# Kernel optimization log

Measured on AMD Instinct MI355X. Metric: run time of the kernel, lower is better.

The kernel has to match this reference:

```python
import jax, jax.numpy as jnp
import numpy as np

B, TQ, TK = 2, 2048, 2048
H, E, D = 16, 256, 4096       # num_heads, embed_dim, d_model
DH = D // H                   # head_dim == embed_dim (required by per-head RMSNorm(embed_dim))
LAMBDA_INIT = 0.8
LAYER_INDEX = 0
EPS = 1.1920929e-07           # torch RMSNorm default eps = finfo(float32).eps


def setup_inputs() -> dict:
    key = jax.random.key(0)
    ks = jax.random.split(key, 14)
    s = 0.02
    lam_init_val = LAMBDA_INIT - 0.6 * float(np.exp(-0.3 * LAYER_INDEX))
    return {
        "x": jax.random.normal(ks[0], (B, TQ, E), jnp.float32),
        "encoder_out": jax.random.normal(ks[1], (B, TK, E), jnp.float32),
        "Wq": jax.random.normal(ks[2], (H, E, DH), jnp.float32) * s,
        "bq": jnp.zeros((H, DH), jnp.float32),
        "Wk": jax.random.normal(ks[3], (H, E, DH), jnp.float32) * s,
        "bk": jnp.zeros((H, DH), jnp.float32),
        "Wv": jax.random.normal(ks[4], (H, E, DH), jnp.float32) * s,
        "bv": jnp.zeros((H, DH), jnp.float32),
        "lq1": jax.random.normal(ks[5], (H, DH), jnp.float32) * 0.1,
        "lk1": jax.random.normal(ks[6], (H, DH), jnp.float32) * 0.1,
        "lq2": jax.random.normal(ks[7], (H, DH), jnp.float32) * 0.1,
        "lk2": jax.random.normal(ks[8], (H, DH), jnp.float32) * 0.1,
        "lam_init": jnp.full((H,), lam_init_val, jnp.float32),
        "g": jnp.ones((H, DH), jnp.float32),     # per-head RMSNorm weight
        "Wo": jax.random.normal(ks[9], (D, E), jnp.float32) * s,
        "bo": jnp.zeros((E,), jnp.float32),
    }


def reference(x, encoder_out, Wq, bq, Wk, bk, Wv, bv,
              lq1, lk1, lq2, lk2, lam_init, g, Wo, bo):
    # per-head projections, vectorized over heads: [B,H,T,DH]
    q = jnp.einsum('bte,hed->bhtd', x, Wq) + bq[:, None, :]
    k = jnp.einsum('bse,hed->bhsd', encoder_out, Wk) + bk[:, None, :]
    v = jnp.einsum('bse,hed->bhsd', encoder_out, Wv) + bv[:, None, :]
    dh2 = DH // 2
    q1, q2 = q[..., :dh2], q[..., dh2:]
    k1, k2 = k[..., :dh2], k[..., dh2:]
    scale = 1.0 / jnp.sqrt(jnp.float32(dh2))
    s1 = jax.nn.softmax(jnp.einsum('bhtd,bhsd->bhts', q1, k1) * scale, axis=-1)
    s2 = jax.nn.softmax(jnp.einsum('bhtd,bhsd->bhts', q2, k2) * scale, axis=-1)
    # learned per-head lambda scalar
    lam = jnp.exp(jnp.sum(lq1 * lk1, axis=-1)) - jnp.exp(jnp.sum(lq2 * lk2, axis=-1)) + lam_init  # [H]
    w = s1 - lam[None, :, None, None] * s2
    o = jnp.einsum('bhts,bhsd->bhtd', w, v)
    # per-head RMSNorm + (1 - lambda_init) scaling
    rms = jnp.sqrt(jnp.mean(o * o, axis=-1, keepdims=True) + EPS)
    o = (1.0 - LAMBDA_INIT) * (o / rms) * g[None, :, None, :]
    # concat heads -> output projection
    o = o.transpose(0, 2, 1, 3).reshape(B, TQ, D)
    return o @ Wo + bo
```

## Files before the change

### kernel.cpp

```cpp
#include <hip/hip_runtime.h>
#include <hip/hip_bf16.h>
#include <stdint.h>
#include <math.h>

typedef __bf16 bf16;
typedef __bf16 bf16x8 __attribute__((ext_vector_type(8)));
typedef float f32x4 __attribute__((ext_vector_type(4)));
typedef float f32x16 __attribute__((ext_vector_type(16)));
typedef unsigned int u32;

#define MFMA16(a, b, c) __builtin_amdgcn_mfma_f32_16x16x32_bf16(a, b, c, 0, 0, 0)
#define MFMA32(a, b, c) __builtin_amdgcn_mfma_f32_32x32x16_bf16(a, b, c, 0, 0, 0)

typedef const u32 __attribute__((address_space(1)))* gptr1;
typedef u32 __attribute__((address_space(3)))* lptr3;

__device__ __forceinline__ void load_lds16(const void* g, void* l) {
    __builtin_amdgcn_global_load_lds((gptr1)g, (lptr3)l, 16, 0, 0);
}

__device__ __forceinline__ u32 pk2(float lo, float hi_) {
    union { bf16 h[2]; u32 u; } t;
    t.h[0] = (bf16)lo; t.h[1] = (bf16)hi_;
    return t.u;
}

#define SCALE_QK 0.08838834764831845f
#define LOG2E 1.4426950408889634f
#define QK_PRESCALE (SCALE_QK * LOG2E)
#define RMS_EPS 1.1920929e-07f
#define OUT_SCALE 0.2f
#define M0_BIAS (-16.0f)

__global__ __launch_bounds__(256) void prep(
    const float* __restrict__ x, const float* __restrict__ enc,
    bf16* __restrict__ xb, bf16* __restrict__ eb,
    const float* __restrict__ Wq, const float* __restrict__ Wk, const float* __restrict__ Wv,
    bf16* __restrict__ WTq, bf16* __restrict__ WTk, bf16* __restrict__ WTv,
    const float* __restrict__ Wo, bf16* __restrict__ WoT,
    const float* __restrict__ lq1, const float* __restrict__ lk1,
    const float* __restrict__ lq2, const float* __restrict__ lk2,
    const float* __restrict__ lam_init, float* __restrict__ lam_out) {
    __shared__ bf16 T[64][68];
    int bid = blockIdx.x, tid = threadIdx.x;

    if (bid < 1024) {
        int gid = bid * 256 + tid;
        const float* src = (gid < 131072) ? x : enc;
        bf16* dst = (gid < 131072) ? xb : eb;
        int i = (gid & 131071) * 8;
        float4 v0 = *(const float4*)(src + i);
        float4 v1 = *(const float4*)(src + i + 4);
        union { bf16 h[8]; uint4 u; } p;
        p.h[0] = (bf16)v0.x; p.h[1] = (bf16)v0.y; p.h[2] = (bf16)v0.z; p.h[3] = (bf16)v0.w;
        p.h[4] = (bf16)v1.x; p.h[5] = (bf16)v1.y; p.h[6] = (bf16)v1.z; p.h[7] = (bf16)v1.w;
        *(uint4*)(dst + i) = p.u;
        return;
    }
    if (bid < 1792) {
        int idx = bid - 1024;
        int z = idx >> 4, rem = idx & 15;
        int by = rem >> 2, bx = rem & 3;
        int iw = z >> 4, hh = z & 15;
        const float* src = (iw == 0 ? Wq : iw == 1 ? Wk : Wv) + hh * 65536;
        bf16* dst = (iw == 0 ? WTq : iw == 1 ? WTk : WTv) + hh * 65536;
        int r0 = by * 64, c0 = bx * 64;
#pragma unroll
        for (int t = 0; t < 4; ++t) {
            int idx2 = tid + t * 256;
            int row = idx2 >> 4, c4 = (idx2 & 15) * 4;
            float4 v = *(const float4*)(src + (r0 + row) * 256 + c0 + c4);
            T[row][c4] = (bf16)v.x; T[row][c4 + 1] = (bf16)v.y;
            T[row][c4 + 2] = (bf16)v.z; T[row][c4 + 3] = (bf16)v.w;
        }
        __syncthreads();
#pragma unroll
        for (int t = 0; t < 2; ++t) {
            int idx2 = tid + t * 256;
            int crow = idx2 >> 3, r8 = (idx2 & 7) * 8;
            union { bf16 h[8]; uint4 u; } p;
#pragma unroll
            for (int j = 0; j < 8; ++j) p.h[j] = T[r8 + j][crow];
            *(uint4*)(dst + (c0 + crow) * 256 + r0 + r8) = p.u;
        }
        return;
    }
    if (bid < 2048) {
        int idx = bid - 1792;
        int by = idx >> 2, bx = idx & 3;
        int r0 = by * 64, c0 = bx * 64;
#pragma unroll
        for (int t = 0; t < 4; ++t) {
            int idx2 = tid + t * 256;
            int row = idx2 >> 4, c4 = (idx2 & 15) * 4;
            float4 v = *(const float4*)(Wo + (size_t)(r0 + row) * 256 + c0 + c4);
            T[row][c4] = (bf16)v.x; T[row][c4 + 1] = (bf16)v.y;
            T[row][c4 + 2] = (bf16)v.z; T[row][c4 + 3] = (bf16)v.w;
        }
        __syncthreads();
#pragma unroll
        for (int t = 0; t < 2; ++t) {
            int idx2 = tid + t * 256;
            int crow = idx2 >> 3, r8 = (idx2 & 7) * 8;
            union { bf16 h[8]; uint4 u; } p;
#pragma unroll
            for (int j = 0; j < 8; ++j) p.h[j] = T[r8 + j][crow];
            *(uint4*)(WoT + (size_t)(c0 + crow) * 4096 + r0 + r8) = p.u;
        }
        return;
    }
    {
        int hh = tid >> 4, i = tid & 15;
        float s1 = 0.f, s2 = 0.f;
#pragma unroll
        for (int j = 0; j < 16; ++j) {
            int d = i + j * 16;
            s1 += lq1[hh * 256 + d] * lk1[hh * 256 + d];
            s2 += lq2[hh * 256 + d] * lk2[hh * 256 + d];
        }
#pragma unroll
        for (int msk = 1; msk < 16; msk <<= 1) { s1 += __shfl_xor(s1, msk); s2 += __shfl_xor(s2, msk); }
        if (i == 0) lam_out[hh] = __expf(s1) - __expf(s2) + lam_init[hh];
    }
}

__global__ __launch_bounds__(256) void proj_gemm(
    const bf16* __restrict__ xb, const bf16* __restrict__ eb,
    const bf16* __restrict__ WTq, const bf16* __restrict__ WTk, const bf16* __restrict__ WTv,
    const float* __restrict__ bq, const float* __restrict__ bk, const float* __restrict__ bv,
    bf16* __restrict__ Qb, bf16* __restrict__ Kb, bf16* __restrict__ VTb) {
    int z = blockIdx.z;
    const bf16* A = (z == 0) ? xb : eb;
    const bf16* BT = (z == 0) ? WTq : (z == 1) ? WTk : WTv;
    const float* bias = (z == 0) ? bq : (z == 1) ? bk : bv;
    bf16* out = (z == 0) ? Qb : Kb;
    float qs = (z == 0) ? QK_PRESCALE : 1.0f;

    __shared__ alignas(16) bf16 As[128 * 64];
    __shared__ alignas(16) bf16 Bs[128 * 64];
    int m0 = blockIdx.x * 128, n0 = blockIdx.y * 128;
    int tid = threadIdx.x, w = tid >> 6, lane = tid & 63;
    int lrow = lane & 15, lgrp = lane >> 4;
    int wr = (w >> 1) * 64, wc = (w & 1) * 64;

    f32x4 acc[4][4];
#pragma unroll
    for (int i = 0; i < 4; ++i)
#pragma unroll
        for (int j = 0; j < 4; ++j) acc[i][j] = (f32x4){0.f, 0.f, 0.f, 0.f};

    for (int k0 = 0; k0 < 256; k0 += 64) {
        __syncthreads();
#pragma unroll
        for (int t = 0; t < 4; ++t) {
            int s = tid + t * 256;
            int row = s >> 3;
            int cg = (s & 7) ^ (row & 7);
            load_lds16(A + (size_t)(m0 + row) * 256 + k0 + cg * 8, &As[s * 8]);
            load_lds16(BT + (size_t)(n0 + row) * 256 + k0 + cg * 8, &Bs[s * 8]);
        }
        __syncthreads();
#pragma unroll
        for (int ks = 0; ks < 2; ++ks) {
            bf16x8 af[4], bfr[4];
#pragma unroll
            for (int f = 0; f < 4; ++f) {
                int ra = wr + f * 16 + lrow;
                int rb = wc + f * 16 + lrow;
                af[f]  = *(const bf16x8*)&As[ra * 64 + (((ks * 4 + lgrp) ^ (ra & 7)) << 3)];
                bfr[f] = *(const bf16x8*)&Bs[rb * 64 + (((ks * 4 + lgrp) ^ (rb & 7)) << 3)];
            }
#pragma unroll
            for (int i = 0; i < 4; ++i)
#pragma unroll
                for (int j = 0; j < 4; ++j) acc[i][j] = MFMA16(af[i], bfr[j], acc[i][j]);
        }
    }

    if (z == 2) {
        int lg2 = ((lgrp & 1) << 1) | (lgrp >> 1);
#pragma unroll
        for (int i = 0; i < 4; ++i) {
            int m_ = m0 + wr + i * 16;
            int bb = m_ >> 11, tb = m_ & 2047;
#pragma unroll
            for (int j = 0; j < 4; ++j) {
                int n = n0 + wc + j * 16 + lrow;
                float bvv = bias[n];
                int hh = n >> 8, d = n & 255;
                union { bf16 h[4]; uint2 u2; } pk;
#pragma unroll
                for (int r = 0; r < 4; ++r) pk.h[r] = (bf16)(acc[i][j][r] + bvv);
                *(uint2*)(VTb + (((size_t)bb * 16 + hh) * 256 + d) * 2048 + tb + lg2 * 4) = pk.u2;
            }
        }
    } else {
#pragma unroll
        for (int i = 0; i < 4; ++i) {
#pragma unroll
            for (int j = 0; j < 4; ++j) {
                int n = n0 + wc + j * 16 + lrow;
                float bvv = bias[n];
                int hh = n >> 8, d = n & 255;
#pragma unroll
                for (int r = 0; r < 4; ++r) {
                    int m = m0 + wr + i * 16 + lgrp * 4 + r;
                    int bb = m >> 11, tt = m & 2047;
                    out[(((size_t)bb * 16 + hh) * 2048 + tt) * 256 + d] = (bf16)((acc[i][j][r] + bvv) * qs);
                }
            }
        }
    }
}

__global__ __launch_bounds__(256, 2) void attn_kernel(
    const bf16* __restrict__ Qb, const bf16* __restrict__ Kb, const bf16* __restrict__ VTb,
    const float* __restrict__ lam_ws, const float* __restrict__ g, bf16* __restrict__ On) {
    __shared__ alignas(16) char SMEM[75264];
    bf16* KsB = (bf16*)SMEM;
    bf16* VsB = (bf16*)(SMEM + 32768);
    float* o2buf  = (float*)SMEM;
    float* smem_i = (float*)(SMEM + 65536);
    float* smem_r = (float*)(SMEM + 66048);
    float* psum   = (float*)(SMEM + 66560);

    int orig = blockIdx.x;
    int xcd = orig & 7, idx = orig >> 3;
    int bh = xcd * 4 + (idx >> 5);
    int qb = idx & 31;
    int b = bh >> 4, h = bh & 15;
    int q0 = qb * 64;

    int tid = threadIdx.x, w = tid >> 6, lane = tid & 63;
    int lq = lane & 31, hi = lane >> 5;
    int br = w >> 1, qw = (w & 1) * 32;
    int ksw = lq & 7;
    int vsw = (lq >> 1) & 3;

    const bf16* Qg = Qb + ((size_t)bh * 2048 + q0 + qw + lq) * 256 + br * 128;
    bf16x8 qf[8];
#pragma unroll
    for (int dk = 0; dk < 8; ++dk)
        qf[dk] = *(const bf16x8*)(Qg + dk * 16 + hi * 8);

    f32x16 o[8];
#pragma unroll
    for (int dt = 0; dt < 8; ++dt)
#pragma unroll
        for (int i = 0; i < 16; ++i) o[dt][i] = 0.f;
    float lsum = 0.f;

    const bf16* Kg = Kb + (size_t)bh * 2048 * 256;
    const bf16* VTg = VTb + (size_t)bh * 256 * 2048;

    auto STAGE = [&](int buf, int kt) {
        int s0 = kt * 32;
#pragma unroll
        for (int i = 0; i < 4; ++i) {
            int s = i * 256 + tid;
            int row = s >> 5;
            int cg = (s & 31) ^ (row & 7);
            load_lds16(Kg + (size_t)(s0 + row) * 256 + cg * 8, KsB + buf * 8192 + s * 8);
        }
#pragma unroll
        for (int i = 0; i < 4; ++i) {
            int s = i * 256 + tid;
            int row = s >> 2;
            int cg = (s & 3) ^ ((row >> 1) & 3);
            load_lds16(VTg + (size_t)row * 2048 + s0 + cg * 8, VsB + buf * 8192 + s * 8);
        }
    };

    STAGE(0, 0);
    __syncthreads();

    int cur = 0;
    for (int kt = 0; kt < 64; ++kt) {
        if (kt + 1 < 64) STAGE(cur ^ 1, kt + 1);
        const bf16* Kbuf = KsB + cur * 8192;
        const bf16* Vbuf = VsB + cur * 8192;

        f32x16 sa, sb;
#pragma unroll
        for (int i = 0; i < 16; ++i) { sa[i] = M0_BIAS; sb[i] = 0.f; }
        __builtin_amdgcn_s_setprio(1);
#pragma unroll
        for (int dk = 0; dk < 4; ++dk) {
            bf16x8 k0 = *(const bf16x8*)&Kbuf[lq * 256 + (((br * 16 + 4 * dk + hi) ^ ksw) << 3)];
            bf16x8 k1 = *(const bf16x8*)&Kbuf[lq * 256 + (((br * 16 + 4 * dk + 2 + hi) ^ ksw) << 3)];
            sa = MFMA32(k0, qf[2 * dk], sa);
            sb = MFMA32(k1, qf[2 * dk + 1], sb);
        }
        __builtin_amdgcn_s_setprio(0);

        float p[16];
        float ls0 = 0.f, ls1 = 0.f;
#pragma unroll
        for (int i = 0; i < 8; ++i) { p[i] = exp2f(sa[i] + sb[i]); ls0 += p[i]; }
#pragma unroll
        for (int i = 8; i < 16; ++i) { p[i] = exp2f(sa[i] + sb[i]); ls1 += p[i]; }
        lsum += ls0 + ls1;

        union { u32 u[4]; bf16x8 v; } PA0, PA1;
        PA0.u[0] = pk2(p[0], p[1]);   PA0.u[1] = pk2(p[2], p[3]);
        PA0.u[2] = pk2(p[4], p[5]);   PA0.u[3] = pk2(p[6], p[7]);
        PA1.u[0] = pk2(p[8], p[9]);   PA1.u[1] = pk2(p[10], p[11]);
        PA1.u[2] = pk2(p[12], p[13]); PA1.u[3] = pk2(p[14], p[15]);

        __builtin_amdgcn_s_setprio(1);
#pragma unroll
        for (int dt = 0; dt < 8; ++dt) {
            const bf16* vrow = &Vbuf[(dt * 32 + lq) * 32];
            bf16x8 v0 = *(const bf16x8*)&vrow[(hi ^ vsw) << 3];
            o[dt] = MFMA32(PA0.v, v0, o[dt]);
            bf16x8 v1 = *(const bf16x8*)&vrow[((2 + hi) ^ vsw) << 3];
            o[dt] = MFMA32(PA1.v, v1, o[dt]);
        }
        __builtin_amdgcn_s_setprio(0);

        __syncthreads();
        cur ^= 1;
    }

    lsum += __shfl_xor(lsum, 32);
    float lam = lam_ws[h];
    float inv = (br == 0) ? 1.f / lsum : lam / lsum;
    smem_i[br * 64 + qw + lq] = inv;
    __syncthreads();

    if (br == 1) {
#pragma unroll
        for (int r = 0; r < 16; ++r) {
            int qp = (r & 3) + 8 * (r >> 2) + 4 * hi + qw;
            float i2 = smem_i[64 + qp];
#pragma unroll
            for (int dt = 0; dt < 8; ++dt)
                o2buf[qp * 256 + dt * 32 + lq] = o[dt][r] * i2;
        }
    }
    __syncthreads();

    if (br == 0) {
#pragma unroll
        for (int r = 0; r < 16; ++r) {
            int qp = (r & 3) + 8 * (r >> 2) + 4 * hi + qw;
            float i1 = smem_i[qp];
            float ss = 0.f;
#pragma unroll
            for (int dt = 0; dt < 8; ++dt) {
                float v = o[dt][r] * i1 - o2buf[qp * 256 + dt * 32 + lq];
                o[dt][r] = v;
                ss += v * v;
            }
            psum[qp * 33 + lq] = ss;
        }
    }
    __syncthreads();

    if (tid < 64) {
        float s = 0.f;
#pragma unroll
        for (int i = 0; i < 32; ++i) s += psum[tid * 33 + i];
        smem_r[tid] = 1.f / sqrtf(s * (1.f / 256.f) + RMS_EPS);
    }
    __syncthreads();

    if (br == 0) {
        float gv[8];
#pragma unroll
        for (int dt = 0; dt < 8; ++dt) gv[dt] = g[h * 256 + dt * 32 + lq] * OUT_SCALE;
#pragma unroll
        for (int r = 0; r < 16; ++r) {
            int qp = (r & 3) + 8 * (r >> 2) + 4 * hi + qw;
            float rv = smem_r[qp];
            size_t base = ((size_t)b * 2048 + q0 + qp) * 4096 + h * 256;
#pragma unroll
            for (int dt = 0; dt < 8; ++dt)
                On[base + dt * 32 + lq] = (bf16)(o[dt][r] * rv * gv[dt]);
        }
    }
}

__global__ __launch_bounds__(256) void out_gemm(const bf16* __restrict__ A, const bf16* __restrict__ BT,
                                                const float* __restrict__ bo, float* __restrict__ out) {
    __shared__ alignas(16) bf16 As[64 * 64];
    __shared__ alignas(16) bf16 Bs[64 * 64];
    int m0 = blockIdx.x * 64, n0 = blockIdx.y * 64;
    int tid = threadIdx.x, w = tid >> 6, lane = tid & 63;
    int lrow = lane & 15, lgrp = lane >> 4;
    int wr = (w >> 1) * 32, wc = (w & 1) * 32;
    f32x4 acc[2][2];
#pragma unroll
    for (int i = 0; i < 2; ++i)
#pragma unroll
        for (int j = 0; j < 2; ++j) acc[i][j] = (f32x4){0.f, 0.f, 0.f, 0.f};
    for (int k0 = 0; k0 < 4096; k0 += 64) {
        __syncthreads();
#pragma unroll
        for (int t = 0; t < 2; ++t) {
            int s = tid + t * 256;
            int row = s >> 3;
            int cg = (s & 7) ^ (row & 7);
            load_lds16(A + (size_t)(m0 + row) * 4096 + k0 + cg * 8, &As[s * 8]);
            load_lds16(BT + (size_t)(n0 + row) * 4096 + k0 + cg * 8, &Bs[s * 8]);
        }
        __syncthreads();
#pragma unroll
        for (int ks = 0; ks < 2; ++ks) {
            bf16x8 af[2], bfr[2];
#pragma unroll
            for (int f = 0; f < 2; ++f) {
                int ra = wr + f * 16 + lrow;
                int rb = wc + f * 16 + lrow;
                af[f]  = *(const bf16x8*)&As[ra * 64 + (((ks * 4 + lgrp) ^ (ra & 7)) << 3)];
                bfr[f] = *(const bf16x8*)&Bs[rb * 64 + (((ks * 4 + lgrp) ^ (rb & 7)) << 3)];
            }
#pragma unroll
            for (int i = 0; i < 2; ++i)
#pragma unroll
                for (int j = 0; j < 2; ++j) acc[i][j] = MFMA16(af[i], bfr[j], acc[i][j]);
        }
    }
#pragma unroll
    for (int i = 0; i < 2; ++i)
#pragma unroll
        for (int j = 0; j < 2; ++j) {
            int n = n0 + wc + j * 16 + lrow;
            float bv = bo[n];
#pragma unroll
            for (int r = 0; r < 4; ++r) {
                int m = m0 + wr + i * 16 + lgrp * 4 + r;
                out[(size_t)m * 256 + n] = acc[i][j][r] + bv;
            }
        }
}

extern "C" void kernel_launch(void* const* d_in, const int* in_sizes, int n_in,
                              void* d_out, int out_size, void* d_ws, size_t ws_size,
                              hipStream_t stream) {
    const float* x = (const float*)d_in[0];
    const float* enc = (const float*)d_in[1];
    const float* Wq = (const float*)d_in[2];
    const float* bq = (const float*)d_in[3];
    const float* Wk = (const float*)d_in[4];
    const float* bk = (const float*)d_in[5];
    const float* Wv = (const float*)d_in[6];
    const float* bv = (const float*)d_in[7];
    const float* lq1 = (const float*)d_in[8];
    const float* lk1 = (const float*)d_in[9];
    const float* lq2 = (const float*)d_in[10];
    const float* lk2 = (const float*)d_in[11];
    const float* lam_init = (const float*)d_in[12];
    const float* g = (const float*)d_in[13];
    const float* Wo = (const float*)d_in[14];
    const float* bo = (const float*)d_in[15];
    float* out = (float*)d_out;

    char* ws = (char*)d_ws;
    const size_t MB = 1024 * 1024;
    bf16* xb  = (bf16*)(ws + 0 * MB);
    bf16* eb  = (bf16*)(ws + 2 * MB);
    bf16* WTq = (bf16*)(ws + 4 * MB);
    bf16* WTk = (bf16*)(ws + 6 * MB);
    bf16* WTv = (bf16*)(ws + 8 * MB);
    bf16* WoT = (bf16*)(ws + 10 * MB);
    float* lam = (float*)(ws + 12 * MB);
    bf16* Qb  = (bf16*)(ws + 13 * MB);
    bf16* Kb  = (bf16*)(ws + 45 * MB);
    bf16* On  = (bf16*)(ws + 77 * MB);
    bf16* VTb = (bf16*)(ws + 109 * MB);

    hipLaunchKernelGGL(prep, dim3(2049), dim3(256), 0, stream,
                       x, enc, xb, eb, Wq, Wk, Wv, WTq, WTk, WTv, Wo, WoT,
                       lq1, lk1, lq2, lk2, lam_init, lam);
    hipLaunchKernelGGL(proj_gemm, dim3(32, 32, 3), dim3(256), 0, stream,
                       xb, eb, WTq, WTk, WTv, bq, bk, bv, Qb, Kb, VTb);
    hipLaunchKernelGGL(attn_kernel, dim3(1024), dim3(256), 0, stream, Qb, Kb, VTb, lam, g, On);
    hipLaunchKernelGGL(out_gemm, dim3(64, 4), dim3(256), 0, stream, On, WoT, bo, out);
}
```

Measured before the change: 329.9 us.

## Shrink attention LDS by single-buffering V and splitting epilogue reduction

After: 333.0 us. Within noise of the previous version (+0.9%).

```diff
diff --git a/kernel.cpp b/kernel.cpp
--- a/kernel.cpp
+++ b/kernel.cpp
@@ -216,13 +216,13 @@
 __global__ __launch_bounds__(256, 2) void attn_kernel(
     const bf16* __restrict__ Qb, const bf16* __restrict__ Kb, const bf16* __restrict__ VTb,
     const float* __restrict__ lam_ws, const float* __restrict__ g, bf16* __restrict__ On) {
-    __shared__ alignas(16) char SMEM[75264];
+    __shared__ alignas(16) char SMEM[49152];
     bf16* KsB = (bf16*)SMEM;
-    bf16* VsB = (bf16*)(SMEM + 32768);
+    bf16* Vs  = (bf16*)(SMEM + 32768);
     float* o2buf  = (float*)SMEM;
-    float* smem_i = (float*)(SMEM + 65536);
-    float* smem_r = (float*)(SMEM + 66048);
-    float* psum   = (float*)(SMEM + 66560);
+    float* smem_i = (float*)(SMEM + 32768);
+    float* smem_r = (float*)(SMEM + 33280);
+    float* psum   = (float*)(SMEM + 33536);
 
     int orig = blockIdx.x;
     int xcd = orig & 7, idx = orig >> 3;
@@ -253,7 +253,7 @@
     const bf16* Kg = Kb + (size_t)bh * 2048 * 256;
     const bf16* VTg = VTb + (size_t)bh * 256 * 2048;
 
-    auto STAGE = [&](int buf, int kt) {
+    auto STAGE_K = [&](int buf, int kt) {
         int s0 = kt * 32;
 #pragma unroll
         for (int i = 0; i < 4; ++i) {
@@ -262,23 +262,30 @@
             int cg = (s & 31) ^ (row & 7);
             load_lds16(Kg + (size_t)(s0 + row) * 256 + cg * 8, KsB + buf * 8192 + s * 8);
         }
+    };
+    auto STAGE_V = [&](int kt) {
+        int s0 = kt * 32;
 #pragma unroll
         for (int i = 0; i < 4; ++i) {
             int s = i * 256 + tid;
             int row = s >> 2;
             int cg = (s & 3) ^ ((row >> 1) & 3);
-            load_lds16(VTg + (size_t)row * 2048 + s0 + cg * 8, VsB + buf * 8192 + s * 8);
+            load_lds16(VTg + (size_t)row * 2048 + s0 + cg * 8, Vs + s * 8);
         }
     };
 
-    STAGE(0, 0);
-    __syncthreads();
-
-    int cur = 0;
+    STAGE_K(0, 0);
+
     for (int kt = 0; kt < 64; ++kt) {
-        if (kt + 1 < 64) STAGE(cur ^ 1, kt + 1);
-        const bf16* Kbuf = KsB + cur * 8192;
-        const bf16* Vbuf = VsB + cur * 8192;
+        asm volatile("s_barrier" ::: "memory");
+        STAGE_V(kt);
+        if (kt + 1 < 64) STAGE_K((kt + 1) & 1, kt + 1);
+
+        if (kt < 63) asm volatile("s_waitcnt vmcnt(8)" ::: "memory");
+        else         asm volatile("s_waitcnt vmcnt(4)" ::: "memory");
+        asm volatile("s_barrier" ::: "memory");
+
+        const bf16* Kbuf = KsB + (kt & 1) * 8192;
 
         f32x16 sa, sb;
 #pragma unroll
@@ -307,20 +314,22 @@
         PA1.u[0] = pk2(p[8], p[9]);   PA1.u[1] = pk2(p[10], p[11]);
         PA1.u[2] = pk2(p[12], p[13]); PA1.u[3] = pk2(p[14], p[15]);
 
+        if (kt < 63) asm volatile("s_waitcnt vmcnt(4)" ::: "memory");
+        else         asm volatile("s_waitcnt vmcnt(0)" ::: "memory");
+        asm volatile("s_barrier" ::: "memory");
+
         __builtin_amdgcn_s_setprio(1);
 #pragma unroll
         for (int dt = 0; dt < 8; ++dt) {
-            const bf16* vrow = &Vbuf[(dt * 32 + lq) * 32];
+            const bf16* vrow = &Vs[(dt * 32 + lq) * 32];
             bf16x8 v0 = *(const bf16x8*)&vrow[(hi ^ vsw) << 3];
             o[dt] = MFMA32(PA0.v, v0, o[dt]);
             bf16x8 v1 = *(const bf16x8*)&vrow[((2 + hi) ^ vsw) << 3];
             o[dt] = MFMA32(PA1.v, v1, o[dt]);
         }
         __builtin_amdgcn_s_setprio(0);
-
-        __syncthreads();
-        cur ^= 1;
-    }
+    }
+    __syncthreads();
 
     lsum += __shfl_xor(lsum, 32);
     float lam = lam_ws[h];
@@ -328,31 +337,44 @@
     smem_i[br * 64 + qw + lq] = inv;
     __syncthreads();
 
-    if (br == 1) {
+    float ssp[16];
+#pragma unroll
+    for (int r = 0; r < 16; ++r) ssp[r] = 0.f;
+
+#pragma unroll
+    for (int half = 0; half < 2; ++half) {
+        if (br == 1) {
+#pragma unroll
+            for (int r = 0; r < 16; ++r) {
+                int qp = (r & 3) + 8 * (r >> 2) + 4 * hi + qw;
+                float i2 = smem_i[64 + qp];
+#pragma unroll
+                for (int d4 = 0; d4 < 4; ++d4)
+                    o2buf[qp * 128 + d4 * 32 + lq] = o[half * 4 + d4][r] * i2;
+            }
+        }
+        __syncthreads();
+        if (br == 0) {
+#pragma unroll
+            for (int r = 0; r < 16; ++r) {
+                int qp = (r & 3) + 8 * (r >> 2) + 4 * hi + qw;
+                float i1 = smem_i[qp];
+#pragma unroll
+                for (int d4 = 0; d4 < 4; ++d4) {
+                    float v = o[half * 4 + d4][r] * i1 - o2buf[qp * 128 + d4 * 32 + lq];
+                    o[half * 4 + d4][r] = v;
+                    ssp[r] += v * v;
+                }
+            }
+        }
+        __syncthreads();
+    }
+
+    if (br == 0) {
 #pragma unroll
         for (int r = 0; r < 16; ++r) {
             int qp = (r & 3) + 8 * (r >> 2) + 4 * hi + qw;
-            float i2 = smem_i[64 + qp];
-#pragma unroll
-            for (int dt = 0; dt < 8; ++dt)
-                o2buf[qp * 256 + dt * 32 + lq] = o[dt][r] * i2;
-        }
-    }
-    __syncthreads();
-
-    if (br == 0) {
-#pragma unroll
-        for (int r = 0; r < 16; ++r) {
-            int qp = (r & 3) + 8 * (r >> 2) + 4 * hi + qw;
-            float i1 = smem_i[qp];
-            float ss = 0.f;
-#pragma unroll
-            for (int dt = 0; dt < 8; ++dt) {
-                float v = o[dt][r] * i1 - o2buf[qp * 256 + dt * 32 + lq];
-                o[dt][r] = v;
-                ss += v * v;
-            }
-            psum[qp * 33 + lq] = ss;
+            psum[qp * 33 + lq] = ssp[r];
         }
     }
     __syncthreads();
```

## Use split-K with atomic accumulation and full-N tiles in output GEMM

Applied to the files above, without the earlier changes.

Measured after the change: 335.4 us. About the same (+1.7%).

```diff
diff --git a/kernel.cpp b/kernel.cpp
--- a/kernel.cpp
+++ b/kernel.cpp
@@ -384,55 +384,57 @@
 __global__ __launch_bounds__(256) void out_gemm(const bf16* __restrict__ A, const bf16* __restrict__ BT,
                                                 const float* __restrict__ bo, float* __restrict__ out) {
     __shared__ alignas(16) bf16 As[64 * 64];
-    __shared__ alignas(16) bf16 Bs[64 * 64];
-    int m0 = blockIdx.x * 64, n0 = blockIdx.y * 64;
+    __shared__ alignas(16) bf16 Bs[256 * 64];
+    int m0 = blockIdx.x * 64;
+    int kz = blockIdx.y;
+    int kbase = kz * 512;
     int tid = threadIdx.x, w = tid >> 6, lane = tid & 63;
     int lrow = lane & 15, lgrp = lane >> 4;
-    int wr = (w >> 1) * 32, wc = (w & 1) * 32;
-    f32x4 acc[2][2];
-#pragma unroll
-    for (int i = 0; i < 2; ++i)
-#pragma unroll
-        for (int j = 0; j < 2; ++j) acc[i][j] = (f32x4){0.f, 0.f, 0.f, 0.f};
-    for (int k0 = 0; k0 < 4096; k0 += 64) {
+    int wr = w * 16;
+
+    f32x4 acc[16];
+#pragma unroll
+    for (int j = 0; j < 16; ++j) acc[j] = (f32x4){0.f, 0.f, 0.f, 0.f};
+
+    for (int k0 = 0; k0 < 512; k0 += 64) {
         __syncthreads();
 #pragma unroll
         for (int t = 0; t < 2; ++t) {
             int s = tid + t * 256;
             int row = s >> 3;
             int cg = (s & 7) ^ (row & 7);
-            load_lds16(A + (size_t)(m0 + row) * 4096 + k0 + cg * 8, &As[s * 8]);
-            load_lds16(BT + (size_t)(n0 + row) * 4096 + k0 + cg * 8, &Bs[s * 8]);
+            load_lds16(A + (size_t)(m0 + row) * 4096 + kbase + k0 + cg * 8, &As[s * 8]);
+        }
+#pragma unroll
+        for (int t = 0; t < 8; ++t) {
+            int s = tid + t * 256;
+            int row = s >> 3;
+            int cg = (s & 7) ^ (row & 7);
+            load_lds16(BT + (size_t)row * 4096 + kbase + k0 + cg * 8, &Bs[s * 8]);
         }
         __syncthreads();
 #pragma unroll
         for (int ks = 0; ks < 2; ++ks) {
-            bf16x8 af[2], bfr[2];
-#pragma unroll
-            for (int f = 0; f < 2; ++f) {
-                int ra = wr + f * 16 + lrow;
-                int rb = wc + f * 16 + lrow;
-                af[f]  = *(const bf16x8*)&As[ra * 64 + (((ks * 4 + lgrp) ^ (ra & 7)) << 3)];
-                bfr[f] = *(const bf16x8*)&Bs[rb * 64 + (((ks * 4 + lgrp) ^ (rb & 7)) << 3)];
+            int ra = wr + lrow;
+            bf16x8 af = *(const bf16x8*)&As[ra * 64 + (((ks * 4 + lgrp) ^ (ra & 7)) << 3)];
+#pragma unroll
+            for (int j = 0; j < 16; ++j) {
+                int rb = j * 16 + lrow;
+                bf16x8 bfr = *(const bf16x8*)&Bs[rb * 64 + (((ks * 4 + lgrp) ^ (rb & 7)) << 3)];
+                acc[j] = MFMA16(af, bfr, acc[j]);
             }
-#pragma unroll
-            for (int i = 0; i < 2; ++i)
-#pragma unroll
-                for (int j = 0; j < 2; ++j) acc[i][j] = MFMA16(af[i], bfr[j], acc[i][j]);
-        }
-    }
-#pragma unroll
-    for (int i = 0; i < 2; ++i)
-#pragma unroll
-        for (int j = 0; j < 2; ++j) {
-            int n = n0 + wc + j * 16 + lrow;
-            float bv = bo[n];
-#pragma unroll
-            for (int r = 0; r < 4; ++r) {
-                int m = m0 + wr + i * 16 + lgrp * 4 + r;
-                out[(size_t)m * 256 + n] = acc[i][j][r] + bv;
-            }
-        }
+        }
+    }
+#pragma unroll
+    for (int j = 0; j < 16; ++j) {
+        int n = j * 16 + lrow;
+        float bv = (kz == 0) ? bo[n] : 0.f;
+#pragma unroll
+        for (int r = 0; r < 4; ++r) {
+            int m = m0 + wr + lgrp * 4 + r;
+            atomicAdd(&out[(size_t)m * 256 + n], acc[j][r] + bv);
+        }
+    }
 }
 
 extern "C" void kernel_launch(void* const* d_in, const int* in_sizes, int n_in,
@@ -470,11 +472,12 @@
     bf16* On  = (bf16*)(ws + 77 * MB);
     bf16* VTb = (bf16*)(ws + 109 * MB);
 
+    hipMemsetAsync(out, 0, (size_t)4096 * 256 * sizeof(float), stream);
     hipLaunchKernelGGL(prep, dim3(2049), dim3(256), 0, stream,
                        x, enc, xb, eb, Wq, Wk, Wv, WTq, WTk, WTv, Wo, WoT,
                        lq1, lk1, lq2, lk2, lam_init, lam);
     hipLaunchKernelGGL(proj_gemm, dim3(32, 32, 3), dim3(256), 0, stream,
                        xb, eb, WTq, WTk, WTv, bq, bk, bv, Qb, Kb, VTb);
     hipLaunchKernelGGL(attn_kernel, dim3(1024), dim3(256), 0, stream, Qb, Kb, VTb, lam, g, On);
-    hipLaunchKernelGGL(out_gemm, dim3(64, 4), dim3(256), 0, stream, On, WoT, bo, out);
-}
+    hipLaunchKernelGGL(out_gemm, dim3(64, 8), dim3(256), 0, stream, On, WoT, bo, out);
+}
```
